# Kernel tuning notes

Measured on AMD Instinct MI355X. Metric: run time of the kernel, lower is better.

The kernel has to match this reference:

```python
import jax, jax.numpy as jnp
import numpy as np

DIM = 768
QK_DIM = 128
HIDDEN = 1536  # expansion_factor 2.0 * dim
B, S = 4, 2048


def setup_inputs() -> dict:
    key = jax.random.key(0)
    ks = jax.random.split(key, 8)
    std = 0.02
    return {
        "hidden_states": jax.random.normal(ks[0], (B, S, DIM), dtype=jnp.float32),
        "attention_mask": jnp.ones((B, S), dtype=bool),
        "ln_gamma": jnp.ones((DIM,), jnp.float32),
        "ln_beta": jnp.zeros((DIM,), jnp.float32),
        "w_hidden": jax.random.normal(ks[1], (DIM, HIDDEN * 2), jnp.float32) * std,
        "b_hidden": jnp.zeros((HIDDEN * 2,), jnp.float32),
        "w_qk": jax.random.normal(ks[2], (DIM, QK_DIM), jnp.float32) * std,
        "b_qk": jnp.zeros((QK_DIM,), jnp.float32),
        "os_gamma": 1.0 + jax.random.normal(ks[3], (2, QK_DIM), jnp.float32) * 0.02,
        "os_beta": jnp.zeros((2, QK_DIM), jnp.float32),
        "w_out": jax.random.normal(ks[4], (HIDDEN, DIM), jnp.float32) * std,
        "b_out": jnp.zeros((DIM,), jnp.float32),
    }


def _layernorm(x, gamma, beta, eps=1e-5):
    mu = jnp.mean(x, axis=-1, keepdims=True)
    var = jnp.mean((x - mu) ** 2, axis=-1, keepdims=True)
    return (x - mu) * jax.lax.rsqrt(var + eps) * gamma + beta


def reference(hidden_states, attention_mask, ln_gamma, ln_beta, w_hidden, b_hidden,
              w_qk, b_qk, os_gamma, os_beta, w_out, b_out):
    seq_len = hidden_states.shape[-2]
    normed = _layernorm(hidden_states, ln_gamma, ln_beta)
    # v / gate branch: Linear -> SiLU -> chunk
    hg = jax.nn.silu(normed @ w_hidden + b_hidden)          # [b, s, 2*hidden]
    v, gate = jnp.split(hg, 2, axis=-1)                     # [b, s, hidden] each
    # qk branch with per-head offset-scale
    qk = jax.nn.silu(normed @ w_qk + b_qk)                  # [b, s, qk_dim]
    q = qk * os_gamma[0] + os_beta[0]
    k = qk * os_gamma[1] + os_beta[1]
    sim = jnp.einsum('bid,bjd->bij', q, k) / seq_len        # [b, s, s]
    attn = jnp.square(jax.nn.relu(sim))                     # relu^2 attention
    attn = jnp.where(attention_mask[:, None, :], attn, 0.0)
    out = jnp.einsum('bij,bjd->bid', attn, v) * gate        # gated AV
    out = out @ w_out + b_out
    return (out + hidden_states,)
```

## Files before the change

kernel.cpp:

```cpp
#include <hip/hip_runtime.h>
#include <hip/hip_bf16.h>
#include <cstdint>
#include <cstddef>

typedef __attribute__((ext_vector_type(8))) __bf16 bf16x8;
typedef __attribute__((ext_vector_type(4))) float f32x4;
typedef __attribute__((ext_vector_type(4))) unsigned short us4;

#define WAITV(N) asm volatile("s_waitcnt vmcnt(" #N ")" ::: "memory")
#define BARRIER() asm volatile("s_barrier" ::: "memory")

__device__ inline unsigned short f2bf(float f) {
    union { float f; unsigned int i; } x; x.f = f;
    unsigned int r = x.i + 0x7fff + ((x.i >> 16) & 1);
    return (unsigned short)(r >> 16);
}
__device__ inline float bf2f(unsigned short u) {
    union { unsigned int i; float f; } x; x.i = ((unsigned int)u) << 16;
    return x.f;
}
__device__ inline float silu(float x) { return x / (1.f + __expf(-x)); }

__global__ __launch_bounds__(256) void tconv_k(const float* __restrict__ src,
                                               unsigned short* __restrict__ dst,
                                               int R, int C) {
    __shared__ float t[32][33];
    int tx = threadIdx.x, ty = threadIdx.y;
    int c0 = blockIdx.x * 32, r0 = blockIdx.y * 32;
#pragma unroll
    for (int i = 0; i < 4; i++)
        t[ty + i * 8][tx] = src[(size_t)(r0 + ty + i * 8) * C + c0 + tx];
    __syncthreads();
#pragma unroll
    for (int i = 0; i < 4; i++)
        dst[(size_t)(c0 + ty + i * 8) * R + r0 + tx] = f2bf(t[tx][ty + i * 8]);
}

__global__ __launch_bounds__(256) void ln_k(const float* __restrict__ x,
                                            const float* __restrict__ gam,
                                            const float* __restrict__ bet,
                                            unsigned short* __restrict__ out) {
    int row = blockIdx.x;
    int tid = threadIdx.x;
    const float* xr = x + (size_t)row * 768;
    float v0 = xr[tid], v1 = xr[tid + 256], v2 = xr[tid + 512];
    float s = v0 + v1 + v2;
    float s2 = v0 * v0 + v1 * v1 + v2 * v2;
#pragma unroll
    for (int m = 1; m < 64; m <<= 1) {
        s += __shfl_xor(s, m, 64);
        s2 += __shfl_xor(s2, m, 64);
    }
    __shared__ float ws[8];
    int wave = tid >> 6, lane = tid & 63;
    if (lane == 0) { ws[wave] = s; ws[4 + wave] = s2; }
    __syncthreads();
    s = ws[0] + ws[1] + ws[2] + ws[3];
    s2 = ws[4] + ws[5] + ws[6] + ws[7];
    float mu = s * (1.f / 768.f);
    float var = s2 * (1.f / 768.f) - mu * mu;
    float rstd = rsqrtf(var + 1e-5f);
    unsigned short* orow = out + (size_t)row * 768;
    orow[tid]       = f2bf((v0 - mu) * rstd * gam[tid]       + bet[tid]);
    orow[tid + 256] = f2bf((v1 - mu) * rstd * gam[tid + 256] + bet[tid + 256]);
    orow[tid + 512] = f2bf((v2 - mu) * rstd * gam[tid + 512] + bet[tid + 512]);
}

struct GArgs {
    const unsigned short* A; const unsigned short* B;
    int lda, ldb, K;
    long long strideAb, strideBb;
    const float* b_hidden; const float* b_qk;
    const float* osg; const float* osb;
    unsigned short *vt, *gate, *q, *k;
    unsigned short* attn;
    float inv_seq;
    const unsigned short* gate_in; unsigned short* a2;
    const float* b_out; const float* resid; float* outf;
};

template <int MODE>
__global__ __launch_bounds__(256, 2) void gemm_k(GArgs g) {
    constexpr int BM = 128, BN = 128, BK = 64;
    __shared__ unsigned short ldsA[2][BM * BK];
    __shared__ unsigned short ldsB[2][BN * BK];

    const int tid = threadIdx.x;
    const int wave = tid >> 6, lane = tid & 63;
    const int wr = wave >> 1, wc = wave & 1;
    const int m0 = blockIdx.x * BM, n0 = blockIdx.y * BN;
    const int b = blockIdx.z;

    const unsigned short* Ab = g.A + (long long)b * g.strideAb;
    const unsigned short* Bb = g.B + (long long)b * g.strideBb;

    const int r8 = lane >> 3;
    const int sl = (lane & 7) ^ r8;

    f32x4 acc[4][4] = {};

    const int lm = lane & 15, lh = lane >> 4;
    const int rowA = wr * 64 + lm;
    const int rowB = wc * 64 + lm;
    const int swz = lane & 7;

    auto stage = [&](int buf, int kt) {
#pragma unroll
        for (int t = 0; t < 4; t++) {
            int ra = wave * 32 + t * 8;
            const unsigned short* ga =
                Ab + (size_t)(m0 + ra + r8) * g.lda + kt * BK + sl * 8;
            __builtin_amdgcn_global_load_lds(
                (const __attribute__((address_space(1))) void*)ga,
                (__attribute__((address_space(3))) void*)&ldsA[buf][ra * BK], 16, 0, 0);
            const unsigned short* gb =
                Bb + (size_t)(n0 + ra + r8) * g.ldb + kt * BK + sl * 8;
            __builtin_amdgcn_global_load_lds(
                (const __attribute__((address_space(1))) void*)gb,
                (__attribute__((address_space(3))) void*)&ldsB[buf][ra * BK], 16, 0, 0);
        }
    };

    stage(0, 0);
    const int nk = g.K / BK;
    for (int kt = 0; kt < nk; ++kt) {
        const int cur = kt & 1;
        if (kt + 1 < nk) {
            stage(cur ^ 1, kt + 1);
            WAITV(8);
        } else {
            WAITV(0);
        }
        BARRIER();

        bf16x8 af[2][4], bf[2][4];
#pragma unroll
        for (int kk = 0; kk < 2; kk++)
#pragma unroll
            for (int m = 0; m < 4; m++)
                af[kk][m] = *(const bf16x8*)&ldsA[cur][(rowA + m * 16) * BK +
                                                      (((kk * 4 + lh) ^ swz) << 3)];
#pragma unroll
        for (int kk = 0; kk < 2; kk++)
#pragma unroll
            for (int n = 0; n < 4; n++)
                bf[kk][n] = *(const bf16x8*)&ldsB[cur][(rowB + n * 16) * BK +
                                                      (((kk * 4 + lh) ^ swz) << 3)];
#pragma unroll
        for (int kk = 0; kk < 2; kk++)
#pragma unroll
            for (int m = 0; m < 4; m++)
#pragma unroll
                for (int n = 0; n < 4; n++)
                    acc[m][n] = __builtin_amdgcn_mfma_f32_16x16x32_bf16(
                        af[kk][m], bf[kk][n], acc[m][n], 0, 0, 0);
        BARRIER();
    }

#pragma unroll
    for (int m = 0; m < 4; m++) {
#pragma unroll
        for (int n = 0; n < 4; n++) {
            f32x4 c = acc[m][n];
            int gm = m0 + wr * 64 + m * 16 + lh * 4;
            int gn = n0 + wc * 64 + n * 16 + lm;
            if constexpr (MODE == 0) {
                float bias = (gn < 3072) ? g.b_hidden[gn] : g.b_qk[gn - 3072];
                float y[4];
#pragma unroll
                for (int r = 0; r < 4; r++) y[r] = silu(c[r] + bias);
                if (gn < 1536) {
                    us4 p;
#pragma unroll
                    for (int r = 0; r < 4; r++) p[r] = f2bf(y[r]);
                    *(us4*)&g.vt[(size_t)gn * 8192 + gm] = p;
                } else if (gn < 3072) {
#pragma unroll
                    for (int r = 0; r < 4; r++)
                        g.gate[(size_t)(gm + r) * 1536 + (gn - 1536)] = f2bf(y[r]);
                } else {
                    int j = gn - 3072;
                    float g0 = g.osg[j], b0 = g.osb[j];
                    float g1 = g.osg[128 + j], b1 = g.osb[128 + j];
#pragma unroll
                    for (int r = 0; r < 4; r++) {
                        g.q[(size_t)(gm + r) * 128 + j] = f2bf(y[r] * g0 + b0);
                        g.k[(size_t)(gm + r) * 128 + j] = f2bf(y[r] * g1 + b1);
                    }
                }
            } else if constexpr (MODE == 1) {
                unsigned short* ab = g.attn + (size_t)b * 2048 * 2048;
#pragma unroll
                for (int r = 0; r < 4; r++) {
                    float p = c[r] * g.inv_seq;
                    p = p > 0.f ? p * p : 0.f;
                    ab[(size_t)(gm + r) * 2048 + gn] = f2bf(p);
                }
            } else if constexpr (MODE == 2) {
#pragma unroll
                for (int r = 0; r < 4; r++) {
                    size_t row = (size_t)b * 2048 + gm + r;
                    float gt = bf2f(g.gate_in[row * 1536 + gn]);
                    g.a2[row * 1536 + gn] = f2bf(c[r] * gt);
                }
            } else {
#pragma unroll
                for (int r = 0; r < 4; r++) {
                    size_t idx = (size_t)(gm + r) * 768 + gn;
                    g.outf[idx] = c[r] + g.b_out[gn] + g.resid[idx];
                }
            }
        }
    }
}

extern "C" void kernel_launch(void* const* d_in, const int* in_sizes, int n_in,
                              void* d_out, int out_size, void* d_ws, size_t ws_size,
                              hipStream_t stream) {
    const float* hidden   = (const float*)d_in[0];
    const float* ln_gamma = (const float*)d_in[2];
    const float* ln_beta  = (const float*)d_in[3];
    const float* w_hidden = (const float*)d_in[4];
    const float* b_hidden = (const float*)d_in[5];
    const float* w_qk     = (const float*)d_in[6];
    const float* b_qk     = (const float*)d_in[7];
    const float* os_gamma = (const float*)d_in[8];
    const float* os_beta  = (const float*)d_in[9];
    const float* w_out    = (const float*)d_in[10];
    const float* b_out    = (const float*)d_in[11];
    float* outp = (float*)d_out;

    char* ws = (char*)d_ws;
    size_t off = 0;
    auto alloc = [&](size_t bytes) {
        size_t o = off;
        off = (off + bytes + 255) & ~(size_t)255;
        return o;
    };
    unsigned short* wT_all = (unsigned short*)(ws + alloc(3200ull * 768 * 2));
    unsigned short* woutT  = (unsigned short*)(ws + alloc(768ull * 1536 * 2));
    unsigned short* vt     = (unsigned short*)(ws + alloc(1536ull * 8192 * 2));
    unsigned short* gate   = (unsigned short*)(ws + alloc(8192ull * 1536 * 2));
    char* bufA = ws + alloc(4ull * 2048 * 2048 * 2);
    char* bufB = ws + alloc(8192ull * 1536 * 2);
    unsigned short* normed = (unsigned short*)bufA;
    unsigned short* attn   = (unsigned short*)bufA;
    unsigned short* qm     = (unsigned short*)bufB;
    unsigned short* km     = (unsigned short*)(bufB + 8192ull * 128 * 2);
    unsigned short* a2     = (unsigned short*)bufB;

    tconv_k<<<dim3(3072 / 32, 768 / 32), dim3(32, 8), 0, stream>>>(w_hidden, wT_all, 768, 3072);
    tconv_k<<<dim3(128 / 32, 768 / 32), dim3(32, 8), 0, stream>>>(w_qk, wT_all + 3072ull * 768, 768, 128);
    tconv_k<<<dim3(768 / 32, 1536 / 32), dim3(32, 8), 0, stream>>>(w_out, woutT, 1536, 768);

    ln_k<<<8192, 256, 0, stream>>>(hidden, ln_gamma, ln_beta, normed);

    GArgs g = {};
    g.inv_seq = 1.f / 2048.f;

    g.A = normed; g.B = wT_all; g.lda = 768; g.ldb = 768; g.K = 768;
    g.strideAb = 0; g.strideBb = 0;
    g.b_hidden = b_hidden; g.b_qk = b_qk; g.osg = os_gamma; g.osb = os_beta;
    g.vt = vt; g.gate = gate; g.q = qm; g.k = km;
    gemm_k<0><<<dim3(64, 25, 1), 256, 0, stream>>>(g);

    GArgs g1 = {};
    g1.A = qm; g1.B = km; g1.lda = 128; g1.ldb = 128; g1.K = 128;
    g1.strideAb = 2048ll * 128; g1.strideBb = 2048ll * 128;
    g1.attn = attn; g1.inv_seq = 1.f / 2048.f;
    gemm_k<1><<<dim3(16, 16, 4), 256, 0, stream>>>(g1);

    GArgs g2 = {};
    g2.A = attn; g2.B = vt; g2.lda = 2048; g2.ldb = 8192; g2.K = 2048;
    g2.strideAb = 2048ll * 2048; g2.strideBb = 2048;
    g2.gate_in = gate; g2.a2 = a2; g2.inv_seq = 1.f / 2048.f;
    gemm_k<2><<<dim3(16, 12, 4), 256, 0, stream>>>(g2);

    GArgs g3 = {};
    g3.A = a2; g3.B = woutT; g3.lda = 1536; g3.ldb = 1536; g3.K = 1536;
    g3.strideAb = 0; g3.strideBb = 0;
    g3.b_out = b_out; g3.resid = hidden; g3.outf = outp;
    gemm_k<3><<<dim3(64, 6, 1), 256, 0, stream>>>(g3);
}
```

Before: 336.2 us.

## Add 256x256-tile eight-wave GEMM with four-stage LDS pipeline for three GEMMs

Introduces a new 512-thread GEMM kernel that uses 256x256 output tiles, BK=32, and a four-slot LDS ring fed by global_load_lds. A and B staging is interleaved between two MFMA half-phases, which run under s_setprio. The input projection, the attention-times-V GEMM and the output projection move to this kernel, while the QK^T GEMM stays on the old 128x128 kernel. The goal is more data reuse per block and better overlap of loads with MFMA work. The cost is far fewer blocks than CUs for some GEMMs (96 and 192 blocks), more LDS per block, and a padded weight buffer whose extra rows are left uninitialized but guarded in the epilogue.

```diff
diff --git a/kernel.cpp b/kernel.cpp
--- a/kernel.cpp
+++ b/kernel.cpp
@@ -8,6 +8,7 @@
 typedef __attribute__((ext_vector_type(4))) unsigned short us4;
 
 #define WAITV(N) asm volatile("s_waitcnt vmcnt(" #N ")" ::: "memory")
+#define WAITL0() asm volatile("s_waitcnt lgkmcnt(0)" ::: "memory")
 #define BARRIER() asm volatile("s_barrier" ::: "memory")
 
 __device__ inline unsigned short f2bf(float f) {
@@ -81,14 +82,14 @@
 
 template <int MODE>
 __global__ __launch_bounds__(256, 2) void gemm_k(GArgs g) {
-    constexpr int BM = 128, BN = 128, BK = 64;
+    constexpr int BM = 128, BK = 64;
     __shared__ unsigned short ldsA[2][BM * BK];
-    __shared__ unsigned short ldsB[2][BN * BK];
+    __shared__ unsigned short ldsB[2][BM * BK];
 
     const int tid = threadIdx.x;
     const int wave = tid >> 6, lane = tid & 63;
     const int wr = wave >> 1, wc = wave & 1;
-    const int m0 = blockIdx.x * BM, n0 = blockIdx.y * BN;
+    const int m0 = blockIdx.x * BM, n0 = blockIdx.y * BM;
     const int b = blockIdx.z;
 
     const unsigned short* Ab = g.A + (long long)b * g.strideAb;
@@ -125,15 +126,11 @@
     const int nk = g.K / BK;
     for (int kt = 0; kt < nk; ++kt) {
         const int cur = kt & 1;
-        if (kt + 1 < nk) {
-            stage(cur ^ 1, kt + 1);
-            WAITV(8);
-        } else {
-            WAITV(0);
-        }
-        BARRIER();
-
-        bf16x8 af[2][4], bf[2][4];
+        if (kt + 1 < nk) { stage(cur ^ 1, kt + 1); WAITV(8); }
+        else { WAITV(0); }
+        BARRIER();
+
+        bf16x8 af[2][4], bfv[2][4];
 #pragma unroll
         for (int kk = 0; kk < 2; kk++)
 #pragma unroll
@@ -144,8 +141,8 @@
         for (int kk = 0; kk < 2; kk++)
 #pragma unroll
             for (int n = 0; n < 4; n++)
-                bf[kk][n] = *(const bf16x8*)&ldsB[cur][(rowB + n * 16) * BK +
-                                                      (((kk * 4 + lh) ^ swz) << 3)];
+                bfv[kk][n] = *(const bf16x8*)&ldsB[cur][(rowB + n * 16) * BK +
+                                                       (((kk * 4 + lh) ^ swz) << 3)];
 #pragma unroll
         for (int kk = 0; kk < 2; kk++)
 #pragma unroll
@@ -153,7 +150,7 @@
 #pragma unroll
                 for (int n = 0; n < 4; n++)
                     acc[m][n] = __builtin_amdgcn_mfma_f32_16x16x32_bf16(
-                        af[kk][m], bf[kk][n], acc[m][n], 0, 0, 0);
+                        af[kk][m], bfv[kk][n], acc[m][n], 0, 0, 0);
         BARRIER();
     }
 
@@ -164,37 +161,159 @@
             f32x4 c = acc[m][n];
             int gm = m0 + wr * 64 + m * 16 + lh * 4;
             int gn = n0 + wc * 64 + n * 16 + lm;
-            if constexpr (MODE == 0) {
-                float bias = (gn < 3072) ? g.b_hidden[gn] : g.b_qk[gn - 3072];
-                float y[4];
-#pragma unroll
-                for (int r = 0; r < 4; r++) y[r] = silu(c[r] + bias);
-                if (gn < 1536) {
-                    us4 p;
-#pragma unroll
-                    for (int r = 0; r < 4; r++) p[r] = f2bf(y[r]);
-                    *(us4*)&g.vt[(size_t)gn * 8192 + gm] = p;
-                } else if (gn < 3072) {
-#pragma unroll
-                    for (int r = 0; r < 4; r++)
-                        g.gate[(size_t)(gm + r) * 1536 + (gn - 1536)] = f2bf(y[r]);
-                } else {
-                    int j = gn - 3072;
-                    float g0 = g.osg[j], b0 = g.osb[j];
-                    float g1 = g.osg[128 + j], b1 = g.osb[128 + j];
-#pragma unroll
-                    for (int r = 0; r < 4; r++) {
-                        g.q[(size_t)(gm + r) * 128 + j] = f2bf(y[r] * g0 + b0);
-                        g.k[(size_t)(gm + r) * 128 + j] = f2bf(y[r] * g1 + b1);
-                    }
-                }
-            } else if constexpr (MODE == 1) {
+            if constexpr (MODE == 1) {
                 unsigned short* ab = g.attn + (size_t)b * 2048 * 2048;
 #pragma unroll
                 for (int r = 0; r < 4; r++) {
                     float p = c[r] * g.inv_seq;
                     p = p > 0.f ? p * p : 0.f;
                     ab[(size_t)(gm + r) * 2048 + gn] = f2bf(p);
+                }
+            }
+        }
+    }
+}
+
+template <int MODE>
+__global__ __launch_bounds__(512, 2) void g256_k(GArgs g) {
+    constexpr int BK = 32;
+    __shared__ unsigned short lds[4][2 * 256 * BK];
+
+    const int tid = threadIdx.x;
+    const int wave = tid >> 6, lane = tid & 63;
+    const int wm = wave >> 2, wn = wave & 3;
+    const int m0 = blockIdx.x * 256, n0 = blockIdx.y * 256;
+    const int b = blockIdx.z;
+
+    const unsigned short* Ab = g.A + (long long)b * g.strideAb;
+    const unsigned short* Bb = g.B + (long long)b * g.strideBb;
+
+    const int srow0 = tid >> 2;
+    const int schunk = tid & 3;
+
+    const int lm = lane & 15, lh = lane >> 4;
+    const int arow0 = wm * 128 + lm;
+    const int brow0 = wn * 64 + lm;
+
+    f32x4 acc[8][4] = {};
+
+    auto stageA = [&](int kt) {
+        int sl = kt & 3;
+#pragma unroll
+        for (int rho = 0; rho < 2; rho++) {
+            int row = rho * 128 + srow0;
+            int cl = schunk ^ ((row >> 1) & 3);
+            const unsigned short* ga = Ab + (size_t)(m0 + row) * g.lda + kt * BK + cl * 8;
+            __builtin_amdgcn_global_load_lds(
+                (const __attribute__((address_space(1))) void*)ga,
+                (__attribute__((address_space(3))) void*)&lds[sl][row * BK + schunk * 8],
+                16, 0, 0);
+        }
+    };
+    auto stageB = [&](int kt) {
+        int sl = kt & 3;
+#pragma unroll
+        for (int rho = 0; rho < 2; rho++) {
+            int row = rho * 128 + srow0;
+            int cl = schunk ^ ((row >> 1) & 3);
+            const unsigned short* gb = Bb + (size_t)(n0 + row) * g.ldb + kt * BK + cl * 8;
+            __builtin_amdgcn_global_load_lds(
+                (const __attribute__((address_space(1))) void*)gb,
+                (__attribute__((address_space(3))) void*)&lds[sl][8192 + row * BK + schunk * 8],
+                16, 0, 0);
+        }
+    };
+
+    const int nk = g.K / BK;
+    stageA(0); stageB(0);
+    stageA(1); stageB(1);
+    stageA(2); stageB(2);
+    WAITV(8);
+    BARRIER();
+
+    for (int kt = 0; kt < nk; ++kt) {
+        const int slot = kt & 3;
+        const unsigned short* As = &lds[slot][0];
+        const unsigned short* Bs = &lds[slot][8192];
+
+        bf16x8 a[4], bv[4];
+#pragma unroll
+        for (int m = 0; m < 4; m++) {
+            int row = arow0 + m * 16;
+            a[m] = *(const bf16x8*)&As[row * BK + ((lh ^ ((row >> 1) & 3)) << 3)];
+        }
+#pragma unroll
+        for (int n = 0; n < 4; n++) {
+            int row = brow0 + n * 16;
+            bv[n] = *(const bf16x8*)&Bs[row * BK + ((lh ^ ((row >> 1) & 3)) << 3)];
+        }
+        if (kt + 3 < nk) stageA(kt + 3);
+        BARRIER();
+        WAITL0();
+        __builtin_amdgcn_sched_barrier(0);
+        __builtin_amdgcn_s_setprio(1);
+#pragma unroll
+        for (int m = 0; m < 4; m++)
+#pragma unroll
+            for (int n = 0; n < 4; n++)
+                acc[m][n] = __builtin_amdgcn_mfma_f32_16x16x32_bf16(a[m], bv[n], acc[m][n], 0, 0, 0);
+        __builtin_amdgcn_s_setprio(0);
+        BARRIER();
+
+#pragma unroll
+        for (int m = 0; m < 4; m++) {
+            int row = arow0 + 64 + m * 16;
+            a[m] = *(const bf16x8*)&As[row * BK + ((lh ^ ((row >> 1) & 3)) << 3)];
+        }
+        if (kt + 3 < nk) stageB(kt + 3);
+        BARRIER();
+        WAITL0();
+        __builtin_amdgcn_sched_barrier(0);
+        __builtin_amdgcn_s_setprio(1);
+#pragma unroll
+        for (int m = 0; m < 4; m++)
+#pragma unroll
+            for (int n = 0; n < 4; n++)
+                acc[m + 4][n] = __builtin_amdgcn_mfma_f32_16x16x32_bf16(a[m], bv[n], acc[m + 4][n], 0, 0, 0);
+        __builtin_amdgcn_s_setprio(0);
+
+        if (kt + 4 <= nk) { WAITV(8); BARRIER(); }
+        else if (kt + 3 == nk) { WAITV(4); BARRIER(); }
+        else if (kt + 2 == nk) { WAITV(0); BARRIER(); }
+    }
+
+#pragma unroll
+    for (int m = 0; m < 8; m++) {
+#pragma unroll
+        for (int n = 0; n < 4; n++) {
+            f32x4 c = acc[m][n];
+            int gm = m0 + wm * 128 + m * 16 + lh * 4;
+            int gn = n0 + wn * 64 + n * 16 + lm;
+            if constexpr (MODE == 0) {
+                if (gn < 3200) {
+                    float bias = (gn < 3072) ? g.b_hidden[gn] : g.b_qk[gn - 3072];
+                    float y[4];
+#pragma unroll
+                    for (int r = 0; r < 4; r++) y[r] = silu(c[r] + bias);
+                    if (gn < 1536) {
+                        us4 p;
+#pragma unroll
+                        for (int r = 0; r < 4; r++) p[r] = f2bf(y[r]);
+                        *(us4*)&g.vt[(size_t)gn * 8192 + gm] = p;
+                    } else if (gn < 3072) {
+#pragma unroll
+                        for (int r = 0; r < 4; r++)
+                            g.gate[(size_t)(gm + r) * 1536 + (gn - 1536)] = f2bf(y[r]);
+                    } else {
+                        int j = gn - 3072;
+                        float g0 = g.osg[j], b0 = g.osb[j];
+                        float g1 = g.osg[128 + j], b1 = g.osb[128 + j];
+#pragma unroll
+                        for (int r = 0; r < 4; r++) {
+                            g.q[(size_t)(gm + r) * 128 + j] = f2bf(y[r] * g0 + b0);
+                            g.k[(size_t)(gm + r) * 128 + j] = f2bf(y[r] * g1 + b1);
+                        }
+                    }
                 }
             } else if constexpr (MODE == 2) {
 #pragma unroll
@@ -237,7 +356,7 @@
         off = (off + bytes + 255) & ~(size_t)255;
         return o;
     };
-    unsigned short* wT_all = (unsigned short*)(ws + alloc(3200ull * 768 * 2));
+    unsigned short* wT_all = (unsigned short*)(ws + alloc(3328ull * 768 * 2));
     unsigned short* woutT  = (unsigned short*)(ws + alloc(768ull * 1536 * 2));
     unsigned short* vt     = (unsigned short*)(ws + alloc(1536ull * 8192 * 2));
     unsigned short* gate   = (unsigned short*)(ws + alloc(8192ull * 1536 * 2));
@@ -256,13 +375,10 @@
     ln_k<<<8192, 256, 0, stream>>>(hidden, ln_gamma, ln_beta, normed);
 
     GArgs g = {};
-    g.inv_seq = 1.f / 2048.f;
-
     g.A = normed; g.B = wT_all; g.lda = 768; g.ldb = 768; g.K = 768;
-    g.strideAb = 0; g.strideBb = 0;
     g.b_hidden = b_hidden; g.b_qk = b_qk; g.osg = os_gamma; g.osb = os_beta;
     g.vt = vt; g.gate = gate; g.q = qm; g.k = km;
-    gemm_k<0><<<dim3(64, 25, 1), 256, 0, stream>>>(g);
+    g256_k<0><<<dim3(32, 13, 1), 512, 0, stream>>>(g);
 
     GArgs g1 = {};
     g1.A = qm; g1.B = km; g1.lda = 128; g1.ldb = 128; g1.K = 128;
@@ -273,12 +389,11 @@
     GArgs g2 = {};
     g2.A = attn; g2.B = vt; g2.lda = 2048; g2.ldb = 8192; g2.K = 2048;
     g2.strideAb = 2048ll * 2048; g2.strideBb = 2048;
-    g2.gate_in = gate; g2.a2 = a2; g2.inv_seq = 1.f / 2048.f;
-    gemm_k<2><<<dim3(16, 12, 4), 256, 0, stream>>>(g2);
+    g2.gate_in = gate; g2.a2 = a2;
+    g256_k<2><<<dim3(8, 6, 4), 512, 0, stream>>>(g2);
 
     GArgs g3 = {};
     g3.A = a2; g3.B = woutT; g3.lda = 1536; g3.ldb = 1536; g3.K = 1536;
-    g3.strideAb = 0; g3.strideBb = 0;
     g3.b_out = b_out; g3.resid = hidden; g3.outf = outp;
-    gemm_k<3><<<dim3(64, 6, 1), 256, 0, stream>>>(g3);
-}
+    g256_k<3><<<dim3(32, 3, 1), 512, 0, stream>>>(g3);
+}
```

Result: slower. 375.6 us (+11.7%).
